# Optimization experiments

Hardware: AMD Instinct MI355X
Metric: run time of the kernel (lower is better)

The kernel has to match this reference:

```python
import jax, jax.numpy as jnp
import numpy as np

D_MODEL, D_K, D_V, H = 1024, 64, 64, 16


def setup_inputs() -> dict:
    key = jax.random.key(0)
    ks = jax.random.split(key, 11)
    b, nq, nk = 2, 2048, 2048
    queries = jax.random.normal(ks[0], (b, nq, D_MODEL), dtype=jnp.float32)
    keys = jax.random.normal(ks[1], (b, nk, D_MODEL), dtype=jnp.float32)
    values = jax.random.normal(ks[2], (b, nk, D_MODEL), dtype=jnp.float32)
    def xavier(k, shape):
        fan_in, fan_out = shape[1], shape[0]
        lim = np.sqrt(6.0 / (fan_in + fan_out)).astype(np.float32)
        return jax.random.uniform(k, shape, jnp.float32, -lim, lim)
    # torch Linear weight shape: (out_features, in_features)
    Wq = xavier(ks[3], (H * D_K, D_MODEL)); bq = jnp.zeros((H * D_K,), jnp.float32)
    Wk = xavier(ks[4], (H * D_K, D_MODEL)); bk = jnp.zeros((H * D_K,), jnp.float32)
    Wv = xavier(ks[5], (H * D_V, D_MODEL)); bv = jnp.zeros((H * D_V,), jnp.float32)
    Wo = xavier(ks[6], (D_MODEL, H * D_V)); bo = jnp.zeros((D_MODEL,), jnp.float32)
    return {"queries": queries, "keys": keys, "values": values,
            "Wq": Wq, "bq": bq, "Wk": Wk, "bk": bk,
            "Wv": Wv, "bv": bv, "Wo": Wo, "bo": bo}


def reference(queries, keys, values, Wq, bq, Wk, bk, Wv, bv, Wo, bo):
    b, nq, _ = queries.shape
    nk = keys.shape[1]
    scale = 1.0 / np.sqrt(D_K).astype(np.float32)
    # projections -> (b, h, n, d)
    q = (queries @ Wq.T + bq).reshape(b, nq, H, D_K).transpose(0, 2, 1, 3)
    k = (keys @ Wk.T + bk).reshape(b, nk, H, D_K).transpose(0, 2, 1, 3)
    v = (values @ Wv.T + bv).reshape(b, nk, H, D_V).transpose(0, 2, 1, 3)
    att = jnp.einsum('bhqd,bhkd->bhqk', q, k) * scale  # (b,h,nq,nk)
    att = jax.nn.softmax(att, axis=-1)
    out = jnp.einsum('bhqk,bhkd->bhqd', att, v)        # (b,h,nq,dv)
    out = out.transpose(0, 2, 1, 3).reshape(b, nq, H * D_V)
    return out @ Wo.T + bo
```

## Files before the change

kernel.cpp:

```cpp
#include <hip/hip_runtime.h>
#include <stdint.h>

typedef __bf16 v8bf __attribute__((ext_vector_type(8)));
typedef float  v4f  __attribute__((ext_vector_type(4)));

#define QSCALE 0.18033688011112042f

typedef __attribute__((address_space(3))) void lds_vp;
typedef const __attribute__((address_space(1))) void gbl_vp;
__device__ __forceinline__ void gl_lds16(const __bf16* g, __bf16* l) {
    __builtin_amdgcn_global_load_lds((gbl_vp*)g, (lds_vp*)l, 16, 0, 0);
}

__device__ __forceinline__ v8bf cvt8(const float* __restrict__ p) {
    float4 x = *reinterpret_cast<const float4*>(p);
    float4 y = *reinterpret_cast<const float4*>(p + 4);
    v8bf r;
    r[0] = (__bf16)x.x; r[1] = (__bf16)x.y; r[2] = (__bf16)x.z; r[3] = (__bf16)x.w;
    r[4] = (__bf16)y.x; r[5] = (__bf16)y.y; r[6] = (__bf16)y.z; r[7] = (__bf16)y.w;
    return r;
}

__global__ __launch_bounds__(256) void cvt_w(
    const float* __restrict__ w0, const float* __restrict__ w1,
    const float* __restrict__ w2, const float* __restrict__ w3,
    __bf16* __restrict__ o0, __bf16* __restrict__ o1,
    __bf16* __restrict__ o2, __bf16* __restrict__ o3)
{
    const float* src; __bf16* dst;
    switch (blockIdx.y) {
        case 0: src = w0; dst = o0; break;
        case 1: src = w1; dst = o1; break;
        case 2: src = w2; dst = o2; break;
        default: src = w3; dst = o3; break;
    }
    size_t i = ((size_t)blockIdx.x * 256 + threadIdx.x) * 8;
    *reinterpret_cast<v8bf*>(dst + i) = cvt8(src + i);
}

__global__ __launch_bounds__(256) void cvt_in(
    const float* __restrict__ i0, const float* __restrict__ i1,
    const float* __restrict__ i2,
    __bf16* __restrict__ o0, __bf16* __restrict__ o1, __bf16* __restrict__ o2)
{
    const float* src; __bf16* dst;
    switch (blockIdx.y) {
        case 0: src = i0; dst = o0; break;
        case 1: src = i1; dst = o1; break;
        default: src = i2; dst = o2; break;
    }
    size_t i = ((size_t)blockIdx.x * 256 + threadIdx.x) * 8;
    *reinterpret_cast<v8bf*>(dst + i) = cvt8(src + i);
}

__device__ __forceinline__ void gemm_body(
    const __bf16* __restrict__ A, const __bf16* __restrict__ W,
    const float* __restrict__ bias, void* __restrict__ outp,
    int mode, float oscale, int bx, int by)
{
    constexpr int K = 1024, N = 1024;
    __shared__ __align__(16) __bf16 As[2][128 * 64];
    __shared__ __align__(16) __bf16 Bs[2][64 * 64];

    const int lane = threadIdx.x & 63;
    const int wave = threadIdx.x >> 6;
    const int quad = lane >> 4;
    const int l15  = lane & 15;
    const int m_base = bx * 128;
    const int n_base = by * 64;
    const int wm = (wave & 1) * 64;
    const int wn = (wave >> 1) * 32;

    int arow[4], acol[4], brow[2], bcol[2];
    #pragma unroll
    for (int i = 0; i < 4; ++i) {
        int L = (i * 4 + wave) * 64 + lane;
        int r = L >> 3, s = L & 7;
        arow[i] = r; acol[i] = (s ^ (r & 7)) * 8;
    }
    #pragma unroll
    for (int i = 0; i < 2; ++i) {
        int L = (i * 4 + wave) * 64 + lane;
        int r = L >> 3, s = L & 7;
        brow[i] = r; bcol[i] = (s ^ (r & 7)) * 8;
    }

    v4f acc[4][2];
    #pragma unroll
    for (int f = 0; f < 4; ++f)
        #pragma unroll
        for (int g = 0; g < 2; ++g) { v4f z = {0.f,0.f,0.f,0.f}; acc[f][g] = z; }

    #pragma unroll
    for (int i = 0; i < 4; ++i)
        gl_lds16(A + (size_t)(m_base + arow[i]) * K + acol[i],
                 &As[0][(i * 4 + wave) * 512]);
    #pragma unroll
    for (int i = 0; i < 2; ++i)
        gl_lds16(W + (size_t)(n_base + brow[i]) * K + bcol[i],
                 &Bs[0][(i * 4 + wave) * 512]);
    __syncthreads();

    for (int it = 0; it < 16; ++it) {
        const int cur = it & 1, nxt = cur ^ 1;
        const int kn = ((it + 1) & 15) * 64;
        #pragma unroll
        for (int i = 0; i < 4; ++i)
            gl_lds16(A + (size_t)(m_base + arow[i]) * K + kn + acol[i],
                     &As[nxt][(i * 4 + wave) * 512]);
        #pragma unroll
        for (int i = 0; i < 2; ++i)
            gl_lds16(W + (size_t)(n_base + brow[i]) * K + kn + bcol[i],
                     &Bs[nxt][(i * 4 + wave) * 512]);

        #pragma unroll
        for (int ks = 0; ks < 2; ++ks) {
            v8bf af[4], bf[2];
            #pragma unroll
            for (int f = 0; f < 4; ++f) {
                const int R = wm + f * 16 + l15;
                const int slot = (ks * 4 + quad) ^ (R & 7);
                af[f] = *reinterpret_cast<const v8bf*>(&As[cur][R * 64 + slot * 8]);
            }
            #pragma unroll
            for (int g = 0; g < 2; ++g) {
                const int R = wn + g * 16 + l15;
                const int slot = (ks * 4 + quad) ^ (R & 7);
                bf[g] = *reinterpret_cast<const v8bf*>(&Bs[cur][R * 64 + slot * 8]);
            }
            #pragma unroll
            for (int f = 0; f < 4; ++f)
                #pragma unroll
                for (int g = 0; g < 2; ++g)
                    acc[f][g] = __builtin_amdgcn_mfma_f32_16x16x32_bf16(
                        af[f], bf[g], acc[f][g], 0, 0, 0);
        }
        __syncthreads();
    }

    #pragma unroll
    for (int f = 0; f < 4; ++f)
        #pragma unroll
        for (int g = 0; g < 2; ++g) {
            const int nc = n_base + wn + g * 16 + l15;
            const float bval = bias[nc];
            #pragma unroll
            for (int r = 0; r < 4; ++r) {
                const int m = m_base + wm + f * 16 + quad * 4 + r;
                const float v = (acc[f][g][r] + bval) * oscale;
                if (mode == 2) {
                    ((float*)outp)[(size_t)m * N + nc] = v;
                } else {
                    int b = m >> 11, n = m & 2047, h = nc >> 6, d = nc & 63;
                    size_t off = (mode == 0)
                        ? ((size_t)(b * 16 + h) * 2048 + n) * 64 + d
                        : ((size_t)(b * 16 + h) * 64 + d) * 2048 + n;
                    ((__bf16*)outp)[off] = (__bf16)v;
                }
            }
        }
}

__global__ __launch_bounds__(256) void qkv_gemm(
    const __bf16* __restrict__ Aq, const __bf16* __restrict__ Ak,
    const __bf16* __restrict__ Av,
    const __bf16* __restrict__ Wq, const __bf16* __restrict__ Wk,
    const __bf16* __restrict__ Wv,
    const float* __restrict__ bq, const float* __restrict__ bk,
    const float* __restrict__ bv,
    __bf16* __restrict__ Qo, __bf16* __restrict__ Ko, __bf16* __restrict__ Vo)
{
    const int id = blockIdx.x;
    const int by = id & 15;
    const int bx = (id >> 4) & 31;
    const int z  = id >> 9;

    const __bf16 *A, *W; const float* bias; __bf16* outp; float oscale; int mode;
    switch (z) {
        case 0:  A = Aq; W = Wq; bias = bq; outp = Qo; oscale = QSCALE; mode = 0; break;
        case 1:  A = Ak; W = Wk; bias = bk; outp = Ko; oscale = 1.0f;   mode = 0; break;
        default: A = Av; W = Wv; bias = bv; outp = Vo; oscale = 1.0f;   mode = 1; break;
    }
    gemm_body(A, W, bias, outp, mode, oscale, bx, by);
}

__global__ __launch_bounds__(256) void out_gemm(
    const __bf16* __restrict__ A, const __bf16* __restrict__ W,
    const float* __restrict__ bias, float* __restrict__ outp)
{
    const int by = blockIdx.x & 15;
    const int bx = blockIdx.x >> 4;
    gemm_body(A, W, bias, outp, 2, 1.0f, bx, by);
}

__global__ __launch_bounds__(256) void attn_kernel(
    const __bf16* __restrict__ Q, const __bf16* __restrict__ Kb_,
    const __bf16* __restrict__ Vt, __bf16* __restrict__ O)
{
    __shared__ __align__(16) __bf16 Ks[2][64 * 64];
    __shared__ __align__(16) __bf16 Vs[2][64 * 64];
    __shared__ __align__(16) __bf16 p_lds[4][2][16][72];

    const int lane = threadIdx.x & 63;
    const int wave = threadIdx.x >> 6;
    const int quad = lane >> 4;
    const int l15  = lane & 15;
    const int bh = blockIdx.x & 31;
    const int qt = blockIdx.x >> 5;
    const int b  = bh >> 4, h = bh & 15;

    const __bf16* Qh = Q   + (size_t)bh * 2048 * 64;
    const __bf16* Kh = Kb_ + (size_t)bh * 2048 * 64;
    const __bf16* Vh = Vt  + (size_t)bh * 64 * 2048;

    int srow[2], scol[2];
    #pragma unroll
    for (int i = 0; i < 2; ++i) {
        int L = (i * 4 + wave) * 64 + lane;
        int r = L >> 3, s = L & 7;
        srow[i] = r; scol[i] = (s ^ (r & 7)) * 8;
    }

    v8bf qf[2][2];
    #pragma unroll
    for (int s = 0; s < 2; ++s)
        #pragma unroll
        for (int ks = 0; ks < 2; ++ks)
            qf[s][ks] = *reinterpret_cast<const v8bf*>(
                Qh + (size_t)(qt * 128 + wave * 32 + s * 16 + l15) * 64 + ks * 32 + quad * 8);

    v4f o_acc[2][4];
    #pragma unroll
    for (int s = 0; s < 2; ++s)
        #pragma unroll
        for (int c = 0; c < 4; ++c) { v4f z = {0.f,0.f,0.f,0.f}; o_acc[s][c] = z; }
    float l_r[2][4];
    #pragma unroll
    for (int s = 0; s < 2; ++s)
        #pragma unroll
        for (int r = 0; r < 4; ++r) l_r[s][r] = 0.f;

    #pragma unroll
    for (int i = 0; i < 2; ++i) {
        gl_lds16(Kh + (size_t)srow[i] * 64 + scol[i], &Ks[0][(i * 4 + wave) * 512]);
        gl_lds16(Vh + (size_t)srow[i] * 2048 + scol[i], &Vs[0][(i * 4 + wave) * 512]);
    }
    __syncthreads();

    for (int kt = 0; kt < 32; ++kt) {
        const int cur = kt & 1, nxt = cur ^ 1;
        const int ktn = (kt + 1) & 31;
        #pragma unroll
        for (int i = 0; i < 2; ++i) {
            gl_lds16(Kh + (size_t)(ktn * 64 + srow[i]) * 64 + scol[i],
                     &Ks[nxt][(i * 4 + wave) * 512]);
            gl_lds16(Vh + (size_t)srow[i] * 2048 + ktn * 64 + scol[i],
                     &Vs[nxt][(i * 4 + wave) * 512]);
        }

        v4f s_t[2][4];
        #pragma unroll
        for (int s = 0; s < 2; ++s)
            #pragma unroll
            for (int c = 0; c < 4; ++c) { v4f z = {0.f,0.f,0.f,0.f}; s_t[s][c] = z; }
        #pragma unroll
        for (int ks = 0; ks < 2; ++ks) {
            v8bf kf[4];
            #pragma unroll
            for (int c = 0; c < 4; ++c) {
                const int R = c * 16 + l15;
                const int slot = (ks * 4 + quad) ^ (R & 7);
                kf[c] = *reinterpret_cast<const v8bf*>(&Ks[cur][R * 64 + slot * 8]);
            }
            #pragma unroll
            for (int c = 0; c < 4; ++c) {
                s_t[0][c] = __builtin_amdgcn_mfma_f32_16x16x32_bf16(qf[0][ks], kf[c], s_t[0][c], 0, 0, 0);
                s_t[1][c] = __builtin_amdgcn_mfma_f32_16x16x32_bf16(qf[1][ks], kf[c], s_t[1][c], 0, 0, 0);
            }
        }

        #pragma unroll
        for (int s = 0; s < 2; ++s)
            #pragma unroll
            for (int r = 0; r < 4; ++r) {
                const float p0 = __builtin_exp2f(s_t[s][0][r]);
                const float p1 = __builtin_exp2f(s_t[s][1][r]);
                const float p2 = __builtin_exp2f(s_t[s][2][r]);
                const float p3 = __builtin_exp2f(s_t[s][3][r]);
                l_r[s][r] += (p0 + p1) + (p2 + p3);
                p_lds[wave][s][quad * 4 + r][0 * 16 + l15] = (__bf16)p0;
                p_lds[wave][s][quad * 4 + r][1 * 16 + l15] = (__bf16)p1;
                p_lds[wave][s][quad * 4 + r][2 * 16 + l15] = (__bf16)p2;
                p_lds[wave][s][quad * 4 + r][3 * 16 + l15] = (__bf16)p3;
            }

        #pragma unroll
        for (int ks = 0; ks < 2; ++ks) {
            v8bf vf[4];
            #pragma unroll
            for (int c = 0; c < 4; ++c) {
                const int R = c * 16 + l15;
                const int slot = (ks * 4 + quad) ^ (R & 7);
                vf[c] = *reinterpret_cast<const v8bf*>(&Vs[cur][R * 64 + slot * 8]);
            }
            #pragma unroll
            for (int s = 0; s < 2; ++s) {
                v8bf pf = *reinterpret_cast<const v8bf*>(&p_lds[wave][s][l15][ks * 32 + quad * 8]);
                #pragma unroll
                for (int c = 0; c < 4; ++c)
                    o_acc[s][c] = __builtin_amdgcn_mfma_f32_16x16x32_bf16(pf, vf[c], o_acc[s][c], 0, 0, 0);
            }
        }
        __syncthreads();
    }

    #pragma unroll
    for (int s = 0; s < 2; ++s)
        #pragma unroll
        for (int r = 0; r < 4; ++r) {
            float l = l_r[s][r];
            #pragma unroll
            for (int off = 1; off < 16; off <<= 1)
                l += __shfl_xor(l, off, 16);
            const float inv_l = 1.0f / l;
            const int qr = qt * 128 + wave * 32 + s * 16 + quad * 4 + r;
            #pragma unroll
            for (int c = 0; c < 4; ++c) {
                const int col = h * 64 + c * 16 + l15;
                O[(size_t)(b * 2048 + qr) * 1024 + col] = (__bf16)(o_acc[s][c][r] * inv_l);
            }
        }
}

extern "C" void kernel_launch(void* const* d_in, const int* in_sizes, int n_in,
                              void* d_out, int out_size, void* d_ws, size_t ws_size,
                              hipStream_t stream) {
    const float* q_in = (const float*)d_in[0];
    const float* k_in = (const float*)d_in[1];
    const float* v_in = (const float*)d_in[2];
    const float* Wq = (const float*)d_in[3];
    const float* bq = (const float*)d_in[4];
    const float* Wk = (const float*)d_in[5];
    const float* bk = (const float*)d_in[6];
    const float* Wv = (const float*)d_in[7];
    const float* bv = (const float*)d_in[8];
    const float* Wo = (const float*)d_in[9];
    const float* bo = (const float*)d_in[10];
    float* out = (float*)d_out;

    __bf16* ws  = (__bf16*)d_ws;
    __bf16* Abq = ws;
    __bf16* Abk = Abq + 4194304;
    __bf16* Abv = Abk + 4194304;
    __bf16* Qb  = Abv + 4194304;
    __bf16* Kb  = Qb  + 4194304;
    __bf16* Vb  = Kb  + 4194304;
    __bf16* Wqb = Vb  + 4194304;
    __bf16* Wkb = Wqb + 1048576;
    __bf16* Wvb = Wkb + 1048576;
    __bf16* Wob = Wvb + 1048576;
    __bf16* Ob  = Abq;

    cvt_w<<<dim3(512, 4), 256, 0, stream>>>(Wq, Wk, Wv, Wo, Wqb, Wkb, Wvb, Wob);
    cvt_in<<<dim3(2048, 3), 256, 0, stream>>>(q_in, k_in, v_in, Abq, Abk, Abv);

    qkv_gemm<<<1536, 256, 0, stream>>>(
        Abq, Abk, Abv, Wqb, Wkb, Wvb, bq, bk, bv, Qb, Kb, Vb);

    attn_kernel<<<512, 256, 0, stream>>>(Qb, Kb, Vb, Ob);

    out_gemm<<<512, 256, 0, stream>>>(Ob, Wob, bo, out);
}
```

Measured before the change: 252.9 us.

## Use 8 waves per attention block and raise MFMA wave priority

The attention kernel moves from 4 waves each handling 32 query rows to 8 waves each handling 16 rows, launched with 512 threads and a launch-bounds occupancy hint. Each thread now issues a single K/V tile load, and per-wave register state is halved. s_setprio is raised around the MFMA blocks in both the attention kernel and the shared GEMM body. The aim is more waves per CU to hide latency, at the cost of each K fragment loaded from LDS being reused across only one query subtile instead of two, which adds LDS traffic.

Result: no change. 248.3 us (-1.8%).

```diff
diff --git a/kernel.cpp b/kernel.cpp
--- a/kernel.cpp
+++ b/kernel.cpp
@@ -128,12 +128,14 @@
                 const int slot = (ks * 4 + quad) ^ (R & 7);
                 bf[g] = *reinterpret_cast<const v8bf*>(&Bs[cur][R * 64 + slot * 8]);
             }
+            __builtin_amdgcn_s_setprio(1);
             #pragma unroll
             for (int f = 0; f < 4; ++f)
                 #pragma unroll
                 for (int g = 0; g < 2; ++g)
                     acc[f][g] = __builtin_amdgcn_mfma_f32_16x16x32_bf16(
                         af[f], bf[g], acc[f][g], 0, 0, 0);
+            __builtin_amdgcn_s_setprio(0);
         }
         __syncthreads();
     }
@@ -193,13 +195,13 @@
     gemm_body(A, W, bias, outp, 2, 1.0f, bx, by);
 }
 
-__global__ __launch_bounds__(256) void attn_kernel(
+__global__ __launch_bounds__(512, 6) void attn_kernel(
     const __bf16* __restrict__ Q, const __bf16* __restrict__ Kb_,
     const __bf16* __restrict__ Vt, __bf16* __restrict__ O)
 {
     __shared__ __align__(16) __bf16 Ks[2][64 * 64];
     __shared__ __align__(16) __bf16 Vs[2][64 * 64];
-    __shared__ __align__(16) __bf16 p_lds[4][2][16][72];
+    __shared__ __align__(16) __bf16 p_lds[8][16][72];
 
     const int lane = threadIdx.x & 63;
     const int wave = threadIdx.x >> 6;
@@ -213,56 +215,34 @@
     const __bf16* Kh = Kb_ + (size_t)bh * 2048 * 64;
     const __bf16* Vh = Vt  + (size_t)bh * 64 * 2048;
 
-    int srow[2], scol[2];
-    #pragma unroll
-    for (int i = 0; i < 2; ++i) {
-        int L = (i * 4 + wave) * 64 + lane;
-        int r = L >> 3, s = L & 7;
-        srow[i] = r; scol[i] = (s ^ (r & 7)) * 8;
-    }
-
-    v8bf qf[2][2];
-    #pragma unroll
-    for (int s = 0; s < 2; ++s)
-        #pragma unroll
-        for (int ks = 0; ks < 2; ++ks)
-            qf[s][ks] = *reinterpret_cast<const v8bf*>(
-                Qh + (size_t)(qt * 128 + wave * 32 + s * 16 + l15) * 64 + ks * 32 + quad * 8);
-
-    v4f o_acc[2][4];
-    #pragma unroll
-    for (int s = 0; s < 2; ++s)
-        #pragma unroll
-        for (int c = 0; c < 4; ++c) { v4f z = {0.f,0.f,0.f,0.f}; o_acc[s][c] = z; }
-    float l_r[2][4];
-    #pragma unroll
-    for (int s = 0; s < 2; ++s)
-        #pragma unroll
-        for (int r = 0; r < 4; ++r) l_r[s][r] = 0.f;
-
-    #pragma unroll
-    for (int i = 0; i < 2; ++i) {
-        gl_lds16(Kh + (size_t)srow[i] * 64 + scol[i], &Ks[0][(i * 4 + wave) * 512]);
-        gl_lds16(Vh + (size_t)srow[i] * 2048 + scol[i], &Vs[0][(i * 4 + wave) * 512]);
-    }
+    const int L    = wave * 64 + lane;
+    const int srow = L >> 3;
+    const int scol = ((L & 7) ^ (srow & 7)) * 8;
+
+    v8bf qf[2];
+    #pragma unroll
+    for (int ks = 0; ks < 2; ++ks)
+        qf[ks] = *reinterpret_cast<const v8bf*>(
+            Qh + (size_t)(qt * 128 + wave * 16 + l15) * 64 + ks * 32 + quad * 8);
+
+    v4f o_acc[4];
+    #pragma unroll
+    for (int c = 0; c < 4; ++c) { v4f z = {0.f,0.f,0.f,0.f}; o_acc[c] = z; }
+    float l_r[4] = {0.f, 0.f, 0.f, 0.f};
+
+    gl_lds16(Kh + (size_t)srow * 64 + scol, &Ks[0][L * 8]);
+    gl_lds16(Vh + (size_t)srow * 2048 + scol, &Vs[0][L * 8]);
     __syncthreads();
 
     for (int kt = 0; kt < 32; ++kt) {
         const int cur = kt & 1, nxt = cur ^ 1;
         const int ktn = (kt + 1) & 31;
-        #pragma unroll
-        for (int i = 0; i < 2; ++i) {
-            gl_lds16(Kh + (size_t)(ktn * 64 + srow[i]) * 64 + scol[i],
-                     &Ks[nxt][(i * 4 + wave) * 512]);
-            gl_lds16(Vh + (size_t)srow[i] * 2048 + ktn * 64 + scol[i],
-                     &Vs[nxt][(i * 4 + wave) * 512]);
-        }
-
-        v4f s_t[2][4];
-        #pragma unroll
-        for (int s = 0; s < 2; ++s)
-            #pragma unroll
-            for (int c = 0; c < 4; ++c) { v4f z = {0.f,0.f,0.f,0.f}; s_t[s][c] = z; }
+        gl_lds16(Kh + (size_t)(ktn * 64 + srow) * 64 + scol, &Ks[nxt][L * 8]);
+        gl_lds16(Vh + (size_t)srow * 2048 + ktn * 64 + scol, &Vs[nxt][L * 8]);
+
+        v4f s_t[4];
+        #pragma unroll
+        for (int c = 0; c < 4; ++c) { v4f z = {0.f,0.f,0.f,0.f}; s_t[c] = z; }
         #pragma unroll
         for (int ks = 0; ks < 2; ++ks) {
             v8bf kf[4];
@@ -272,27 +252,25 @@
                 const int slot = (ks * 4 + quad) ^ (R & 7);
                 kf[c] = *reinterpret_cast<const v8bf*>(&Ks[cur][R * 64 + slot * 8]);
             }
-            #pragma unroll
-            for (int c = 0; c < 4; ++c) {
-                s_t[0][c] = __builtin_amdgcn_mfma_f32_16x16x32_bf16(qf[0][ks], kf[c], s_t[0][c], 0, 0, 0);
-                s_t[1][c] = __builtin_amdgcn_mfma_f32_16x16x32_bf16(qf[1][ks], kf[c], s_t[1][c], 0, 0, 0);
-            }
-        }
-
-        #pragma unroll
-        for (int s = 0; s < 2; ++s)
-            #pragma unroll
-            for (int r = 0; r < 4; ++r) {
-                const float p0 = __builtin_exp2f(s_t[s][0][r]);
-                const float p1 = __builtin_exp2f(s_t[s][1][r]);
-                const float p2 = __builtin_exp2f(s_t[s][2][r]);
-                const float p3 = __builtin_exp2f(s_t[s][3][r]);
-                l_r[s][r] += (p0 + p1) + (p2 + p3);
-                p_lds[wave][s][quad * 4 + r][0 * 16 + l15] = (__bf16)p0;
-                p_lds[wave][s][quad * 4 + r][1 * 16 + l15] = (__bf16)p1;
-                p_lds[wave][s][quad * 4 + r][2 * 16 + l15] = (__bf16)p2;
-                p_lds[wave][s][quad * 4 + r][3 * 16 + l15] = (__bf16)p3;
-            }
+            __builtin_amdgcn_s_setprio(1);
+            #pragma unroll
+            for (int c = 0; c < 4; ++c)
+                s_t[c] = __builtin_amdgcn_mfma_f32_16x16x32_bf16(qf[ks], kf[c], s_t[c], 0, 0, 0);
+            __builtin_amdgcn_s_setprio(0);
+        }
+
+        #pragma unroll
+        for (int r = 0; r < 4; ++r) {
+            const float p0 = __builtin_exp2f(s_t[0][r]);
+            const float p1 = __builtin_exp2f(s_t[1][r]);
+            const float p2 = __builtin_exp2f(s_t[2][r]);
+            const float p3 = __builtin_exp2f(s_t[3][r]);
+            l_r[r] += (p0 + p1) + (p2 + p3);
+            p_lds[wave][quad * 4 + r][0 * 16 + l15] = (__bf16)p0;
+            p_lds[wave][quad * 4 + r][1 * 16 + l15] = (__bf16)p1;
+            p_lds[wave][quad * 4 + r][2 * 16 + l15] = (__bf16)p2;
+            p_lds[wave][quad * 4 + r][3 * 16 + l15] = (__bf16)p3;
+        }
 
         #pragma unroll
         for (int ks = 0; ks < 2; ++ks) {
@@ -303,33 +281,31 @@
                 const int slot = (ks * 4 + quad) ^ (R & 7);
                 vf[c] = *reinterpret_cast<const v8bf*>(&Vs[cur][R * 64 + slot * 8]);
             }
-            #pragma unroll
-            for (int s = 0; s < 2; ++s) {
-                v8bf pf = *reinterpret_cast<const v8bf*>(&p_lds[wave][s][l15][ks * 32 + quad * 8]);
-                #pragma unroll
-                for (int c = 0; c < 4; ++c)
-                    o_acc[s][c] = __builtin_amdgcn_mfma_f32_16x16x32_bf16(pf, vf[c], o_acc[s][c], 0, 0, 0);
-            }
+            const v8bf pf = *reinterpret_cast<const v8bf*>(
+                &p_lds[wave][l15][ks * 32 + quad * 8]);
+            __builtin_amdgcn_s_setprio(1);
+            #pragma unroll
+            for (int c = 0; c < 4; ++c)
+                o_acc[c] = __builtin_amdgcn_mfma_f32_16x16x32_bf16(pf, vf[c], o_acc[c], 0, 0, 0);
+            __builtin_amdgcn_s_setprio(0);
         }
         __syncthreads();
     }
 
     #pragma unroll
-    for (int s = 0; s < 2; ++s)
-        #pragma unroll
-        for (int r = 0; r < 4; ++r) {
-            float l = l_r[s][r];
-            #pragma unroll
-            for (int off = 1; off < 16; off <<= 1)
-                l += __shfl_xor(l, off, 16);
-            const float inv_l = 1.0f / l;
-            const int qr = qt * 128 + wave * 32 + s * 16 + quad * 4 + r;
-            #pragma unroll
-            for (int c = 0; c < 4; ++c) {
-                const int col = h * 64 + c * 16 + l15;
-                O[(size_t)(b * 2048 + qr) * 1024 + col] = (__bf16)(o_acc[s][c][r] * inv_l);
-            }
-        }
+    for (int r = 0; r < 4; ++r) {
+        float l = l_r[r];
+        #pragma unroll
+        for (int off = 1; off < 16; off <<= 1)
+            l += __shfl_xor(l, off, 16);
+        const float inv_l = 1.0f / l;
+        const int qr = qt * 128 + wave * 16 + quad * 4 + r;
+        #pragma unroll
+        for (int c = 0; c < 4; ++c) {
+            const int col = h * 64 + c * 16 + l15;
+            O[(size_t)(b * 2048 + qr) * 1024 + col] = (__bf16)(o_acc[c][r] * inv_l);
+        }
+    }
 }
 
 extern "C" void kernel_launch(void* const* d_in, const int* in_sizes, int n_in,
@@ -367,7 +343,7 @@
     qkv_gemm<<<1536, 256, 0, stream>>>(
         Abq, Abk, Abv, Wqb, Wkb, Wvb, bq, bk, bv, Qb, Kb, Vb);
 
-    attn_kernel<<<512, 256, 0, stream>>>(Qb, Kb, Vb, Ob);
+    attn_kernel<<<512, 512, 0, stream>>>(Qb, Kb, Vb, Ob);
 
     out_gemm<<<512, 256, 0, stream>>>(Ob, Wob, bo, out);
 }
```

## Rewrite attention inner loop with 32x32 MFMA and register-resident P

Applied to the files above, without the earlier changes.

The attention kernel now computes S^T with 32x32x16 MFMAs so each lane holds a full column of probabilities. It converts them to bf16 with packed converts and rearranges them through permlane32 swaps, so P goes straight into the PV MFMA without passing through LDS. K/V staging becomes triple-buffered with explicit vmcnt waits and raw barriers instead of __syncthreads, and MFMA blocks are wrapped in s_setprio in both the attention and GEMM kernels. The aim is to remove the LDS round trip for P and hide more global-load latency. The cost is more LDS per block, a launch-bounds occupancy hint, and hand-written inline asm whose correctness depends on the MFMA lane layout.

Measured after the change: 245.1 us. -3.1%, faster.

```diff
diff --git a/kernel.cpp b/kernel.cpp
--- a/kernel.cpp
+++ b/kernel.cpp
@@ -3,6 +3,9 @@
 
 typedef __bf16 v8bf __attribute__((ext_vector_type(8)));
 typedef float  v4f  __attribute__((ext_vector_type(4)));
+typedef float  v16f __attribute__((ext_vector_type(16)));
+typedef unsigned int u32;
+typedef unsigned int v4u __attribute__((ext_vector_type(4)));
 
 #define QSCALE 0.18033688011112042f
 
@@ -10,6 +13,15 @@
 typedef const __attribute__((address_space(1))) void gbl_vp;
 __device__ __forceinline__ void gl_lds16(const __bf16* g, __bf16* l) {
     __builtin_amdgcn_global_load_lds((gbl_vp*)g, (lds_vp*)l, 16, 0, 0);
+}
+
+__device__ __forceinline__ u32 cvtpk(float a, float b) {
+    u32 r;
+    asm("v_cvt_pk_bf16_f32 %0, %1, %2" : "=v"(r) : "v"(a), "v"(b));
+    return r;
+}
+__device__ __forceinline__ void swapl(u32& x, u32& y) {
+    asm("v_permlane32_swap_b32 %0, %1" : "+v"(x), "+v"(y));
 }
 
 __device__ __forceinline__ v8bf cvt8(const float* __restrict__ p) {
@@ -128,12 +140,14 @@
                 const int slot = (ks * 4 + quad) ^ (R & 7);
                 bf[g] = *reinterpret_cast<const v8bf*>(&Bs[cur][R * 64 + slot * 8]);
             }
+            __builtin_amdgcn_s_setprio(1);
             #pragma unroll
             for (int f = 0; f < 4; ++f)
                 #pragma unroll
                 for (int g = 0; g < 2; ++g)
                     acc[f][g] = __builtin_amdgcn_mfma_f32_16x16x32_bf16(
                         af[f], bf[g], acc[f][g], 0, 0, 0);
+            __builtin_amdgcn_s_setprio(0);
         }
         __syncthreads();
     }
@@ -193,18 +207,18 @@
     gemm_body(A, W, bias, outp, 2, 1.0f, bx, by);
 }
 
-__global__ __launch_bounds__(256) void attn_kernel(
+__global__ __launch_bounds__(256, 2) void attn_kernel(
     const __bf16* __restrict__ Q, const __bf16* __restrict__ Kb_,
     const __bf16* __restrict__ Vt, __bf16* __restrict__ O)
 {
-    __shared__ __align__(16) __bf16 Ks[2][64 * 64];
-    __shared__ __align__(16) __bf16 Vs[2][64 * 64];
-    __shared__ __align__(16) __bf16 p_lds[4][2][16][72];
+    __shared__ __align__(16) __bf16 Ks[3][64 * 64];
+    __shared__ __align__(16) __bf16 Vs[3][64 * 64];
+    __shared__ float l_lds[4][32];
 
     const int lane = threadIdx.x & 63;
     const int wave = threadIdx.x >> 6;
-    const int quad = lane >> 4;
-    const int l15  = lane & 15;
+    const int l31  = lane & 31;
+    const int hi   = lane >> 5;
     const int bh = blockIdx.x & 31;
     const int qt = blockIdx.x >> 5;
     const int b  = bh >> 4, h = bh & 15;
@@ -221,114 +235,121 @@
         srow[i] = r; scol[i] = (s ^ (r & 7)) * 8;
     }
 
-    v8bf qf[2][2];
-    #pragma unroll
-    for (int s = 0; s < 2; ++s)
-        #pragma unroll
-        for (int ks = 0; ks < 2; ++ks)
-            qf[s][ks] = *reinterpret_cast<const v8bf*>(
-                Qh + (size_t)(qt * 128 + wave * 32 + s * 16 + l15) * 64 + ks * 32 + quad * 8);
-
-    v4f o_acc[2][4];
-    #pragma unroll
-    for (int s = 0; s < 2; ++s)
-        #pragma unroll
-        for (int c = 0; c < 4; ++c) { v4f z = {0.f,0.f,0.f,0.f}; o_acc[s][c] = z; }
-    float l_r[2][4];
-    #pragma unroll
-    for (int s = 0; s < 2; ++s)
-        #pragma unroll
-        for (int r = 0; r < 4; ++r) l_r[s][r] = 0.f;
+    const int qrow = qt * 128 + wave * 32 + l31;
+    v8bf qf[4];
+    #pragma unroll
+    for (int t = 0; t < 4; ++t)
+        qf[t] = *reinterpret_cast<const v8bf*>(
+            Qh + (size_t)qrow * 64 + t * 16 + hi * 8);
+    asm volatile("s_waitcnt vmcnt(0)" ::: "memory");
+
+    v16f o_acc[2];
+    #pragma unroll
+    for (int nt = 0; nt < 2; ++nt)
+        #pragma unroll
+        for (int r = 0; r < 16; ++r) o_acc[nt][r] = 0.f;
+    float l_r = 0.f;
 
     #pragma unroll
     for (int i = 0; i < 2; ++i) {
         gl_lds16(Kh + (size_t)srow[i] * 64 + scol[i], &Ks[0][(i * 4 + wave) * 512]);
         gl_lds16(Vh + (size_t)srow[i] * 2048 + scol[i], &Vs[0][(i * 4 + wave) * 512]);
     }
-    __syncthreads();
-
+    #pragma unroll
+    for (int i = 0; i < 2; ++i) {
+        gl_lds16(Kh + (size_t)(64 + srow[i]) * 64 + scol[i], &Ks[1][(i * 4 + wave) * 512]);
+        gl_lds16(Vh + (size_t)srow[i] * 2048 + 64 + scol[i], &Vs[1][(i * 4 + wave) * 512]);
+    }
+    asm volatile("s_waitcnt vmcnt(4)" ::: "memory");
+    __builtin_amdgcn_s_barrier();
+
+    int cur = 0;
     for (int kt = 0; kt < 32; ++kt) {
-        const int cur = kt & 1, nxt = cur ^ 1;
-        const int ktn = (kt + 1) & 31;
+        int pre = cur + 2; if (pre >= 3) pre -= 3;
+        int ktn = kt + 2; if (ktn >= 32) ktn -= 32;
         #pragma unroll
         for (int i = 0; i < 2; ++i) {
             gl_lds16(Kh + (size_t)(ktn * 64 + srow[i]) * 64 + scol[i],
-                     &Ks[nxt][(i * 4 + wave) * 512]);
+                     &Ks[pre][(i * 4 + wave) * 512]);
             gl_lds16(Vh + (size_t)srow[i] * 2048 + ktn * 64 + scol[i],
-                     &Vs[nxt][(i * 4 + wave) * 512]);
-        }
-
-        v4f s_t[2][4];
-        #pragma unroll
-        for (int s = 0; s < 2; ++s)
-            #pragma unroll
-            for (int c = 0; c < 4; ++c) { v4f z = {0.f,0.f,0.f,0.f}; s_t[s][c] = z; }
-        #pragma unroll
-        for (int ks = 0; ks < 2; ++ks) {
+                     &Vs[pre][(i * 4 + wave) * 512]);
+        }
+
+        v16f st[2];
+        #pragma unroll
+        for (int kb = 0; kb < 2; ++kb)
+            #pragma unroll
+            for (int r = 0; r < 16; ++r) st[kb][r] = 0.f;
+        #pragma unroll
+        for (int kb = 0; kb < 2; ++kb) {
+            const int R = kb * 32 + l31;
             v8bf kf[4];
             #pragma unroll
-            for (int c = 0; c < 4; ++c) {
-                const int R = c * 16 + l15;
-                const int slot = (ks * 4 + quad) ^ (R & 7);
-                kf[c] = *reinterpret_cast<const v8bf*>(&Ks[cur][R * 64 + slot * 8]);
+            for (int t = 0; t < 4; ++t) {
+                const int slot = (2 * t + hi) ^ (R & 7);
+                kf[t] = *reinterpret_cast<const v8bf*>(&Ks[cur][R * 64 + slot * 8]);
             }
-            #pragma unroll
-            for (int c = 0; c < 4; ++c) {
-                s_t[0][c] = __builtin_amdgcn_mfma_f32_16x16x32_bf16(qf[0][ks], kf[c], s_t[0][c], 0, 0, 0);
-                s_t[1][c] = __builtin_amdgcn_mfma_f32_16x16x32_bf16(qf[1][ks], kf[c], s_t[1][c], 0, 0, 0);
-            }
-        }
-
-        #pragma unroll
-        for (int s = 0; s < 2; ++s)
-            #pragma unroll
-            for (int r = 0; r < 4; ++r) {
-                const float p0 = __builtin_exp2f(s_t[s][0][r]);
-                const float p1 = __builtin_exp2f(s_t[s][1][r]);
-                const float p2 = __builtin_exp2f(s_t[s][2][r]);
-                const float p3 = __builtin_exp2f(s_t[s][3][r]);
-                l_r[s][r] += (p0 + p1) + (p2 + p3);
-                p_lds[wave][s][quad * 4 + r][0 * 16 + l15] = (__bf16)p0;
-                p_lds[wave][s][quad * 4 + r][1 * 16 + l15] = (__bf16)p1;
-                p_lds[wave][s][quad * 4 + r][2 * 16 + l15] = (__bf16)p2;
-                p_lds[wave][s][quad * 4 + r][3 * 16 + l15] = (__bf16)p3;
-            }
-
-        #pragma unroll
-        for (int ks = 0; ks < 2; ++ks) {
-            v8bf vf[4];
-            #pragma unroll
-            for (int c = 0; c < 4; ++c) {
-                const int R = c * 16 + l15;
-                const int slot = (ks * 4 + quad) ^ (R & 7);
-                vf[c] = *reinterpret_cast<const v8bf*>(&Vs[cur][R * 64 + slot * 8]);
-            }
-            #pragma unroll
-            for (int s = 0; s < 2; ++s) {
-                v8bf pf = *reinterpret_cast<const v8bf*>(&p_lds[wave][s][l15][ks * 32 + quad * 8]);
+            __builtin_amdgcn_s_setprio(1);
+            #pragma unroll
+            for (int t = 0; t < 4; ++t)
+                st[kb] = __builtin_amdgcn_mfma_f32_32x32x16_bf16(
+                    kf[t], qf[t], st[kb], 0, 0, 0);
+            __builtin_amdgcn_s_setprio(0);
+        }
+
+        v8bf pa[2][2];
+        #pragma unroll
+        for (int kb = 0; kb < 2; ++kb) {
+            float p[16];
+            #pragma unroll
+            for (int r = 0; r < 16; ++r) p[r] = __builtin_exp2f(st[kb][r]);
+            #pragma unroll
+            for (int r = 0; r < 16; ++r) l_r += p[r];
+            u32 w0 = cvtpk(p[0],  p[1]),  w1 = cvtpk(p[2],  p[3]);
+            u32 w2 = cvtpk(p[4],  p[5]),  w3 = cvtpk(p[6],  p[7]);
+            u32 w4 = cvtpk(p[8],  p[9]),  w5 = cvtpk(p[10], p[11]);
+            u32 w6 = cvtpk(p[12], p[13]), w7 = cvtpk(p[14], p[15]);
+            swapl(w0, w2); swapl(w1, w3);
+            swapl(w4, w6); swapl(w5, w7);
+            v4u t0; t0.x = w0; t0.y = w1; t0.z = w2; t0.w = w3;
+            v4u t1; t1.x = w4; t1.y = w5; t1.z = w6; t1.w = w7;
+            pa[kb][0] = __builtin_bit_cast(v8bf, t0);
+            pa[kb][1] = __builtin_bit_cast(v8bf, t1);
+        }
+
+        #pragma unroll
+        for (int nt = 0; nt < 2; ++nt) {
+            const int R = nt * 32 + l31;
+            #pragma unroll
+            for (int kb = 0; kb < 2; ++kb)
                 #pragma unroll
-                for (int c = 0; c < 4; ++c)
-                    o_acc[s][c] = __builtin_amdgcn_mfma_f32_16x16x32_bf16(pf, vf[c], o_acc[s][c], 0, 0, 0);
-            }
-        }
-        __syncthreads();
-    }
-
-    #pragma unroll
-    for (int s = 0; s < 2; ++s)
-        #pragma unroll
-        for (int r = 0; r < 4; ++r) {
-            float l = l_r[s][r];
-            #pragma unroll
-            for (int off = 1; off < 16; off <<= 1)
-                l += __shfl_xor(l, off, 16);
-            const float inv_l = 1.0f / l;
-            const int qr = qt * 128 + wave * 32 + s * 16 + quad * 4 + r;
-            #pragma unroll
-            for (int c = 0; c < 4; ++c) {
-                const int col = h * 64 + c * 16 + l15;
-                O[(size_t)(b * 2048 + qr) * 1024 + col] = (__bf16)(o_acc[s][c][r] * inv_l);
-            }
+                for (int s = 0; s < 2; ++s) {
+                    const int slot = (kb * 4 + 2 * s + hi) ^ (R & 7);
+                    v8bf vb = *reinterpret_cast<const v8bf*>(
+                        &Vs[cur][R * 64 + slot * 8]);
+                    __builtin_amdgcn_s_setprio(1);
+                    o_acc[nt] = __builtin_amdgcn_mfma_f32_32x32x16_bf16(
+                        pa[kb][s], vb, o_acc[nt], 0, 0, 0);
+                    __builtin_amdgcn_s_setprio(0);
+                }
+        }
+
+        asm volatile("s_waitcnt vmcnt(4)" ::: "memory");
+        __builtin_amdgcn_s_barrier();
+        cur = (cur == 2) ? 0 : cur + 1;
+    }
+
+    float lt = l_r + __shfl_xor(l_r, 32);
+    float inv = 1.0f / lt;
+    if (lane < 32) l_lds[wave][l31] = inv;
+    #pragma unroll
+    for (int nt = 0; nt < 2; ++nt)
+        #pragma unroll
+        for (int r = 0; r < 16; ++r) {
+            const int qloc = (r & 3) + 8 * (r >> 2) + 4 * hi;
+            const int q = qt * 128 + wave * 32 + qloc;
+            const float v = o_acc[nt][r] * l_lds[wave][qloc];
+            O[(size_t)(b * 2048 + q) * 1024 + h * 64 + nt * 32 + l31] = (__bf16)v;
         }
 }
 
```
